# Kernel optimization log

Measured on AMD Instinct MI355X. Metric: run time of the kernel, lower is better.

Reference implementation:

```python
import jax, jax.numpy as jnp
import numpy as np

B, C, H, W = 8, 512, 64, 64
D = C // 8  # 64

def setup_inputs() -> dict:
    key = jax.random.key(0)
    ks = jax.random.split(key, 10)
    s = 0.02
    return {
        "x":  jax.random.normal(ks[0], (B, C, H, W), dtype=jnp.float32),
        "Wq": jax.random.normal(ks[1], (D, C), dtype=jnp.float32) * s,
        "bq": jnp.zeros((D,), dtype=jnp.float32),
        "Wk": jax.random.normal(ks[2], (D, C), dtype=jnp.float32) * s,
        "bk": jnp.zeros((D,), dtype=jnp.float32),
        "Wv": jax.random.normal(ks[3], (D, C), dtype=jnp.float32) * s,
        "bv": jnp.zeros((D,), dtype=jnp.float32),
        "Wo": jax.random.normal(ks[4], (C, D), dtype=jnp.float32) * s,
        "bo": jnp.zeros((C,), dtype=jnp.float32),
        "gamma": jnp.full((1,), 0.5, dtype=jnp.float32),
    }

def reference(x, Wq, bq, Wk, bk, Wv, bv, Wo, bo, gamma):
    b, c, h, w = x.shape
    n = h * w
    xf = x.reshape(b, c, n)                                   # (B, C, N)
    # 1x1 convs == channel matmuls (spectral_norm only reparametrizes the weight)
    q = jnp.einsum('dc,bcn->bnd', Wq, xf) + bq                # (B, N, D)
    k = jnp.einsum('dc,bcn->bdn', Wk, xf) + bk[:, None]       # (B, D, N)
    v = jnp.einsum('dc,bcn->bdn', Wv, xf) + bv[:, None]       # (B, D, N)
    # unscaled scores, softmax over key index (last dim)
    attn = jax.nn.softmax(jnp.einsum('bnd,bdm->bnm', q, k), axis=-1)  # (B, N, N)
    out = jnp.einsum('bdm,bnm->bdn', v, attn)                 # (B, D, N)
    out = jnp.einsum('cd,bdn->bcn', Wo, out) + bo[:, None]    # (B, C, N)
    return (out * gamma + xf).reshape(b, c, h, w)
```

## Files before the change

kernel.cpp:

```cpp
#include <hip/hip_runtime.h>

#define DEVFN __device__ __forceinline__

typedef __bf16 bf16x8 __attribute__((ext_vector_type(8)));
typedef float f32x4 __attribute__((ext_vector_type(4)));
typedef float float4_t __attribute__((ext_vector_type(4)));
typedef unsigned short ushort8_t __attribute__((ext_vector_type(8)));
typedef unsigned short ushort4_t __attribute__((ext_vector_type(4)));

constexpr int Bd = 8, Cd = 512, Nd = 4096, Dd = 64;

DEVFN unsigned short f2bf(float f) {
    union { float f; unsigned int u; } v; v.f = f;
    unsigned int r = (v.u + 0x7FFFu + ((v.u >> 16) & 1u)) >> 16;
    return (unsigned short)r;
}

DEVFN bf16x8 ld_bf8(const unsigned short* p) {
    ushort8_t u = *(const ushort8_t*)p;
    return __builtin_bit_cast(bf16x8, u);
}

DEVFN f32x4 mfma16(bf16x8 a, bf16x8 b, f32x4 c) {
    return __builtin_amdgcn_mfma_f32_16x16x32_bf16(a, b, c, 0, 0, 0);
}

__global__ __launch_bounds__(256) void k_cvtw(
    const float* __restrict__ Wq, const float* __restrict__ Wk,
    const float* __restrict__ Wv, const float* __restrict__ Wo,
    unsigned short* __restrict__ w4)
{
    int i = blockIdx.x * 256 + threadIdx.x;
    w4[i]          = f2bf(Wq[i]);
    w4[32768 + i]  = f2bf(Wk[i]);
    w4[65536 + i]  = f2bf(Wv[i]);
    w4[98304 + i]  = f2bf(Wo[i]);
}

__global__ __launch_bounds__(256) void k_qkv(
    const float* __restrict__ x,
    const unsigned short* __restrict__ wq,
    const unsigned short* __restrict__ wk,
    const unsigned short* __restrict__ wv,
    const float* __restrict__ bq, const float* __restrict__ bk, const float* __restrict__ bv,
    unsigned short* __restrict__ q_nd, unsigned short* __restrict__ k_nd,
    unsigned short* __restrict__ v_dn)
{
    const int b   = blockIdx.y;
    const int n0  = blockIdx.x * 64;
    const int tid = threadIdx.x, wid = tid >> 6, l = tid & 63;
    const int lo  = l & 15, hi = l >> 4;
    const int n0w = n0 + wid * 16;
    const float* xb = x + (size_t)b * Cd * Nd;

    __shared__ unsigned short t_lds[4][16][72];
    __shared__ unsigned short vt_s[64][72];

    f32x4 accq[4] = {}, acck[4] = {}, accv[4] = {};

    for (int c0 = 0; c0 < Cd; c0 += 32) {
        ushort8_t ux;
        #pragma unroll
        for (int j = 0; j < 8; ++j)
            ux[j] = f2bf(xb[(size_t)(c0 + hi * 8 + j) * Nd + n0w + lo]);
        bf16x8 bx = __builtin_bit_cast(bf16x8, ux);
        #pragma unroll
        for (int ds = 0; ds < 4; ++ds) {
            const int wrow = (ds * 16 + lo) * Cd + c0 + hi * 8;
            accq[ds] = mfma16(ld_bf8(wq + wrow), bx, accq[ds]);
            acck[ds] = mfma16(ld_bf8(wk + wrow), bx, acck[ds]);
            accv[ds] = mfma16(ld_bf8(wv + wrow), bx, accv[ds]);
        }
    }

    const int row = l >> 2, dg = l & 3;

    #pragma unroll
    for (int ds = 0; ds < 4; ++ds) {
        ushort4_t u4;
        #pragma unroll
        for (int r = 0; r < 4; ++r) u4[r] = f2bf(accq[ds][r] + bq[ds*16 + hi*4 + r]);
        *(ushort4_t*)&t_lds[wid][lo][ds*16 + hi*4] = u4;
    }
    __syncthreads();
    {
        ushort8_t a0 = *(const ushort8_t*)&t_lds[wid][row][dg*16];
        ushort8_t a1 = *(const ushort8_t*)&t_lds[wid][row][dg*16 + 8];
        unsigned short* dst = q_nd + ((size_t)b * Nd + n0 + wid*16 + row) * 64 + dg*16;
        *(ushort8_t*)dst = a0; *(ushort8_t*)(dst + 8) = a1;
    }
    __syncthreads();

    #pragma unroll
    for (int ds = 0; ds < 4; ++ds) {
        ushort4_t u4;
        #pragma unroll
        for (int r = 0; r < 4; ++r) u4[r] = f2bf(acck[ds][r] + bk[ds*16 + hi*4 + r]);
        *(ushort4_t*)&t_lds[wid][lo][ds*16 + hi*4] = u4;
    }
    __syncthreads();
    {
        ushort8_t a0 = *(const ushort8_t*)&t_lds[wid][row][dg*16];
        ushort8_t a1 = *(const ushort8_t*)&t_lds[wid][row][dg*16 + 8];
        unsigned short* dst = k_nd + ((size_t)b * Nd + n0 + wid*16 + row) * 64 + dg*16;
        *(ushort8_t*)dst = a0; *(ushort8_t*)(dst + 8) = a1;
    }
    __syncthreads();

    #pragma unroll
    for (int ds = 0; ds < 4; ++ds) {
        #pragma unroll
        for (int r = 0; r < 4; ++r)
            vt_s[ds*16 + hi*4 + r][wid*16 + lo] = f2bf(accv[ds][r] + bv[ds*16 + hi*4 + r]);
    }
    __syncthreads();
    {
        const int d = tid >> 2, ng = tid & 3;
        ushort8_t a0 = *(const ushort8_t*)&vt_s[d][ng*16];
        ushort8_t a1 = *(const ushort8_t*)&vt_s[d][ng*16 + 8];
        unsigned short* dst = v_dn + ((size_t)b * Dd + d) * Nd + n0 + ng*16;
        *(ushort8_t*)dst = a0; *(ushort8_t*)(dst + 8) = a1;
    }
}

__global__ __launch_bounds__(256, 2) void k_attn(
    const unsigned short* __restrict__ q_nd,
    const unsigned short* __restrict__ k_nd,
    const unsigned short* __restrict__ v_dn,
    unsigned short* __restrict__ o_nd)
{
    const int bid = blockIdx.x;
    const int b   = bid & 7;
    const int n0  = (bid >> 3) * 64;
    const int tid = threadIdx.x, wid = tid >> 6, l = tid & 63;
    const int lo  = l & 15, hi = l >> 4;
    const int n0w = n0 + wid * 16;
    const int lsw = lo & 7;

    __shared__ unsigned short k_tile[64 * 64];
    __shared__ unsigned short v_tile[64 * 64];
    __shared__ unsigned short p_lds[4][16][72];

    const unsigned short* qb = q_nd + (size_t)b * Nd * Dd;
    const unsigned short* kb = k_nd + (size_t)b * Nd * Dd;
    const unsigned short* vb = v_dn + (size_t)b * Dd * Nd;

    bf16x8 aq[2];
    #pragma unroll
    for (int kc = 0; kc < 2; ++kc)
        aq[kc] = ld_bf8(qb + (size_t)(n0w + lo) * 64 + kc*32 + hi*8);

    f32x4 acc[4] = {};
    float l_st[4] = {0.f, 0.f, 0.f, 0.f};

    const int sr = tid >> 3, ss = tid & 7;
    const int wsl = (ss ^ (sr & 7)) * 8;
    ushort8_t kr0, kr1, vr0, vr1;

    auto gload = [&](int t) {
        const size_t m1 = (size_t)t * 64;
        kr0 = *(const ushort8_t*)(kb + (m1 + sr) * 64 + ss * 8);
        kr1 = *(const ushort8_t*)(kb + (m1 + 32 + sr) * 64 + ss * 8);
        vr0 = *(const ushort8_t*)(vb + (size_t)sr * Nd + m1 + ss * 8);
        vr1 = *(const ushort8_t*)(vb + (size_t)(32 + sr) * Nd + m1 + ss * 8);
    };
    auto dswrite = [&]() {
        *(ushort8_t*)(k_tile + sr * 64 + wsl)        = kr0;
        *(ushort8_t*)(k_tile + (32 + sr) * 64 + wsl) = kr1;
        *(ushort8_t*)(v_tile + sr * 64 + wsl)        = vr0;
        *(ushort8_t*)(v_tile + (32 + sr) * 64 + wsl) = vr1;
    };

    auto compute = [&]() {
        f32x4 s[4] = {};
        #pragma unroll
        for (int ms = 0; ms < 4; ++ms) {
            #pragma unroll
            for (int kc = 0; kc < 2; ++kc) {
                bf16x8 kf = ld_bf8(k_tile + (ms*16 + lo) * 64 + (((kc*4 + hi) ^ lsw) * 8));
                s[ms] = mfma16(aq[kc], kf, s[ms]);
            }
        }
        float p[4][4];
        #pragma unroll
        for (int ms = 0; ms < 4; ++ms) {
            #pragma unroll
            for (int r = 0; r < 4; ++r)
                p[ms][r] = __expf(s[ms][r]);
        }
        #pragma unroll
        for (int r = 0; r < 4; ++r)
            l_st[r] += (p[0][r] + p[1][r]) + (p[2][r] + p[3][r]);
        #pragma unroll
        for (int ms = 0; ms < 4; ++ms) {
            #pragma unroll
            for (int r = 0; r < 4; ++r)
                p_lds[wid][hi*4 + r][ms*16 + lo] = f2bf(p[ms][r]);
        }
        asm volatile("" ::: "memory");
        bf16x8 ap0 = ld_bf8(&p_lds[wid][lo][0*32 + hi*8]);
        bf16x8 ap1 = ld_bf8(&p_lds[wid][lo][1*32 + hi*8]);
        #pragma unroll
        for (int ds = 0; ds < 4; ++ds) {
            bf16x8 vf0 = ld_bf8(v_tile + (ds*16 + lo) * 64 + (((0*4 + hi) ^ lsw) * 8));
            acc[ds] = mfma16(ap0, vf0, acc[ds]);
            bf16x8 vf1 = ld_bf8(v_tile + (ds*16 + lo) * 64 + (((1*4 + hi) ^ lsw) * 8));
            acc[ds] = mfma16(ap1, vf1, acc[ds]);
        }
    };

    constexpr int NT = Nd / 64;
    gload(0);
    dswrite();
    __syncthreads();
    for (int t = 0; t < NT - 1; ++t) {
        gload(t + 1);
        __builtin_amdgcn_sched_barrier(0);
        compute();
        __syncthreads();
        dswrite();
        __syncthreads();
    }
    compute();

    float lr[4];
    #pragma unroll
    for (int r = 0; r < 4; ++r) {
        float ps = l_st[r];
        #pragma unroll
        for (int off = 1; off < 16; off <<= 1)
            ps += __shfl_xor(ps, off, 64);
        lr[r] = ps;
    }
    #pragma unroll
    for (int ds = 0; ds < 4; ++ds) {
        #pragma unroll
        for (int r = 0; r < 4; ++r) {
            float o = acc[ds][r] / lr[r];
            o_nd[((size_t)b * Nd + n0w + hi*4 + r) * 64 + ds*16 + lo] = f2bf(o);
        }
    }
}

__global__ __launch_bounds__(256) void k_oproj(
    const unsigned short* __restrict__ o_nd,
    const unsigned short* __restrict__ wo,
    const float* __restrict__ bo,
    const float* __restrict__ gamma,
    const float* __restrict__ x,
    float* __restrict__ out)
{
    const int b   = blockIdx.y;
    const int n0  = blockIdx.x * 64;
    const int tid = threadIdx.x, wid = tid >> 6, l = tid & 63;
    const int lo  = l & 15, hi = l >> 4;
    const int n0w = n0 + wid * 16;
    const float g = gamma[0];

    bf16x8 ao[2];
    #pragma unroll
    for (int kc = 0; kc < 2; ++kc)
        ao[kc] = ld_bf8(o_nd + ((size_t)b * Nd + n0w + lo) * 64 + kc*32 + hi*8);

    for (int ct = 0; ct < 32; ++ct) {
        f32x4 acc = {};
        #pragma unroll
        for (int kc = 0; kc < 2; ++kc) {
            bf16x8 bw = ld_bf8(wo + (ct*16 + lo) * 64 + kc*32 + hi*8);
            acc = mfma16(ao[kc], bw, acc);
        }
        const int c = ct*16 + lo;
        const float bc = bo[c];
        const size_t base = ((size_t)b * Cd + c) * Nd + n0w + hi*4;
        float4_t xv = *(const float4_t*)(x + base);
        float4_t ov;
        #pragma unroll
        for (int r = 0; r < 4; ++r) ov[r] = g * (acc[r] + bc) + xv[r];
        *(float4_t*)(out + base) = ov;
    }
}

extern "C" void kernel_launch(void* const* d_in, const int* in_sizes, int n_in,
                              void* d_out, int out_size, void* d_ws, size_t ws_size,
                              hipStream_t stream) {
    (void)in_sizes; (void)n_in; (void)out_size; (void)ws_size;
    const float* x  = (const float*)d_in[0];
    const float* Wq = (const float*)d_in[1];
    const float* bq = (const float*)d_in[2];
    const float* Wk = (const float*)d_in[3];
    const float* bk = (const float*)d_in[4];
    const float* Wv = (const float*)d_in[5];
    const float* bv = (const float*)d_in[6];
    const float* Wo = (const float*)d_in[7];
    const float* bo = (const float*)d_in[8];
    const float* gm = (const float*)d_in[9];
    float* out = (float*)d_out;

    unsigned short* w4   = (unsigned short*)d_ws;
    unsigned short* q_nd = w4 + 131072;
    unsigned short* k_nd = q_nd + (size_t)Bd * Nd * Dd;
    unsigned short* v_dn = k_nd + (size_t)Bd * Nd * Dd;
    unsigned short* o_nd = v_dn + (size_t)Bd * Nd * Dd;

    k_cvtw<<<128, 256, 0, stream>>>(Wq, Wk, Wv, Wo, w4);
    dim3 g1(Nd / 64, Bd);
    k_qkv<<<g1, 256, 0, stream>>>(x, w4, w4 + 32768, w4 + 65536, bq, bk, bv, q_nd, k_nd, v_dn);
    k_attn<<<512, 256, 0, stream>>>(q_nd, k_nd, v_dn, o_nd);
    k_oproj<<<g1, 256, 0, stream>>>(o_nd, w4 + 98304, bo, gm, x, out);
}
```

Measured before the change: 169.0 us.

## Restructure attention kernel: register-resident P, 2x2 wave split, double-buffered K/V

Splits the four waves into a 2x2 grid over query halves and key halves, so each K fragment read from LDS feeds two query sub-tiles. Computes S transposed so the exponentiated probabilities can be packed directly into the MFMA A-operand in registers, which removes the P round trip through LDS. Double-buffers the K/V tiles to drop one barrier per iteration, stores V with a permuted swizzle to match the new fragment layout, and adds an LDS cross-wave reduction of partial outputs and row sums at the end. This costs more registers for accumulators and extra LDS for the reduction buffers, which may lower occupancy.

```diff
diff --git a/kernel.cpp b/kernel.cpp
--- a/kernel.cpp
+++ b/kernel.cpp
@@ -1,4 +1,5 @@
 #include <hip/hip_runtime.h>
+#include <hip/hip_bf16.h>
 
 #define DEVFN __device__ __forceinline__
 
@@ -7,6 +8,7 @@
 typedef float float4_t __attribute__((ext_vector_type(4)));
 typedef unsigned short ushort8_t __attribute__((ext_vector_type(8)));
 typedef unsigned short ushort4_t __attribute__((ext_vector_type(4)));
+typedef unsigned int uint4_t __attribute__((ext_vector_type(4)));
 
 constexpr int Bd = 8, Cd = 512, Nd = 4096, Dd = 64;
 
@@ -14,6 +16,12 @@
     union { float f; unsigned int u; } v; v.f = f;
     unsigned int r = (v.u + 0x7FFFu + ((v.u >> 16) & 1u)) >> 16;
     return (unsigned short)r;
+}
+
+DEVFN unsigned int pack2(float a, float b) {
+    __hip_bfloat162 h = __float22bfloat162_rn(make_float2(a, b));
+    union { __hip_bfloat162 h; unsigned int u; } c; c.h = h;
+    return c.u;
 }
 
 DEVFN bf16x8 ld_bf8(const unsigned short* p) {
@@ -134,27 +142,36 @@
     const int n0  = (bid >> 3) * 64;
     const int tid = threadIdx.x, wid = tid >> 6, l = tid & 63;
     const int lo  = l & 15, hi = l >> 4;
-    const int n0w = n0 + wid * 16;
     const int lsw = lo & 7;
-
-    __shared__ unsigned short k_tile[64 * 64];
-    __shared__ unsigned short v_tile[64 * 64];
-    __shared__ unsigned short p_lds[4][16][72];
+    const int qh  = wid >> 1;
+    const int kh  = wid & 1;
+    const int wk0 = kh * 32;
+
+    __shared__ unsigned short k_tiles[2][64 * 64];
+    __shared__ unsigned short v_tiles[2][64 * 64];
+    __shared__ float red_acc[2][2][4][256];
+    __shared__ float red_l[2][2][16];
 
     const unsigned short* qb = q_nd + (size_t)b * Nd * Dd;
     const unsigned short* kb = k_nd + (size_t)b * Nd * Dd;
     const unsigned short* vb = v_dn + (size_t)b * Dd * Nd;
 
-    bf16x8 aq[2];
-    #pragma unroll
-    for (int kc = 0; kc < 2; ++kc)
-        aq[kc] = ld_bf8(qb + (size_t)(n0w + lo) * 64 + kc*32 + hi*8);
-
-    f32x4 acc[4] = {};
-    float l_st[4] = {0.f, 0.f, 0.f, 0.f};
+    bf16x8 aq[2][2];
+    #pragma unroll
+    for (int qs = 0; qs < 2; ++qs)
+        #pragma unroll
+        for (int kc = 0; kc < 2; ++kc)
+            aq[qs][kc] = ld_bf8(qb + (size_t)(n0 + qh*32 + qs*16 + lo) * 64 + kc*32 + hi*8);
+
+    f32x4 acc[2][4] = {};
+    float l_p[2] = {0.f, 0.f};
 
     const int sr = tid >> 3, ss = tid & 7;
-    const int wsl = (ss ^ (sr & 7)) * 8;
+    const int kwsl = (ss ^ (sr & 7)) * 8;
+    const int vkh = ss >> 2, vsl = ss & 3, vms = vsl >> 1;
+    const int vg0 = vkh * 4 + ((2 * vsl) & 3);
+    const int vg1 = vkh * 4 + ((2 * vsl + 1) & 3);
+    const int vsw = sr & 7;
     ushort8_t kr0, kr1, vr0, vr1;
 
     auto gload = [&](int t) {
@@ -164,80 +181,109 @@
         vr0 = *(const ushort8_t*)(vb + (size_t)sr * Nd + m1 + ss * 8);
         vr1 = *(const ushort8_t*)(vb + (size_t)(32 + sr) * Nd + m1 + ss * 8);
     };
-    auto dswrite = [&]() {
-        *(ushort8_t*)(k_tile + sr * 64 + wsl)        = kr0;
-        *(ushort8_t*)(k_tile + (32 + sr) * 64 + wsl) = kr1;
-        *(ushort8_t*)(v_tile + sr * 64 + wsl)        = vr0;
-        *(ushort8_t*)(v_tile + (32 + sr) * 64 + wsl) = vr1;
+    auto dswrite = [&](int buf) {
+        unsigned short* kt = k_tiles[buf];
+        unsigned short* vt = v_tiles[buf];
+        *(ushort8_t*)(kt + sr * 64 + kwsl)        = kr0;
+        *(ushort8_t*)(kt + (32 + sr) * 64 + kwsl) = kr1;
+        ushort4_t a0 = __builtin_shufflevector(vr0, vr0, 0, 1, 2, 3);
+        ushort4_t a1 = __builtin_shufflevector(vr0, vr0, 4, 5, 6, 7);
+        ushort4_t b0 = __builtin_shufflevector(vr1, vr1, 0, 1, 2, 3);
+        ushort4_t b1 = __builtin_shufflevector(vr1, vr1, 4, 5, 6, 7);
+        *(ushort4_t*)(vt + sr * 64 + (vg0 ^ vsw) * 8 + vms * 4)        = a0;
+        *(ushort4_t*)(vt + sr * 64 + (vg1 ^ vsw) * 8 + vms * 4)        = a1;
+        *(ushort4_t*)(vt + (32 + sr) * 64 + (vg0 ^ vsw) * 8 + vms * 4) = b0;
+        *(ushort4_t*)(vt + (32 + sr) * 64 + (vg1 ^ vsw) * 8 + vms * 4) = b1;
     };
 
-    auto compute = [&]() {
-        f32x4 s[4] = {};
-        #pragma unroll
-        for (int ms = 0; ms < 4; ++ms) {
+    auto compute = [&](int buf) {
+        const unsigned short* kt = k_tiles[buf];
+        const unsigned short* vt = v_tiles[buf];
+        f32x4 s[2][2] = {};
+        #pragma unroll
+        for (int ms = 0; ms < 2; ++ms) {
             #pragma unroll
             for (int kc = 0; kc < 2; ++kc) {
-                bf16x8 kf = ld_bf8(k_tile + (ms*16 + lo) * 64 + (((kc*4 + hi) ^ lsw) * 8));
-                s[ms] = mfma16(aq[kc], kf, s[ms]);
+                bf16x8 kf = ld_bf8(kt + (wk0 + ms*16 + lo) * 64 + (((kc*4 + hi) ^ lsw) * 8));
+                #pragma unroll
+                for (int qs = 0; qs < 2; ++qs)
+                    s[qs][ms] = mfma16(kf, aq[qs][kc], s[qs][ms]);
             }
         }
-        float p[4][4];
-        #pragma unroll
-        for (int ms = 0; ms < 4; ++ms) {
-            #pragma unroll
-            for (int r = 0; r < 4; ++r)
-                p[ms][r] = __expf(s[ms][r]);
-        }
-        #pragma unroll
-        for (int r = 0; r < 4; ++r)
-            l_st[r] += (p[0][r] + p[1][r]) + (p[2][r] + p[3][r]);
-        #pragma unroll
-        for (int ms = 0; ms < 4; ++ms) {
-            #pragma unroll
-            for (int r = 0; r < 4; ++r)
-                p_lds[wid][hi*4 + r][ms*16 + lo] = f2bf(p[ms][r]);
-        }
-        asm volatile("" ::: "memory");
-        bf16x8 ap0 = ld_bf8(&p_lds[wid][lo][0*32 + hi*8]);
-        bf16x8 ap1 = ld_bf8(&p_lds[wid][lo][1*32 + hi*8]);
-        #pragma unroll
-        for (int ds = 0; ds < 4; ++ds) {
-            bf16x8 vf0 = ld_bf8(v_tile + (ds*16 + lo) * 64 + (((0*4 + hi) ^ lsw) * 8));
-            acc[ds] = mfma16(ap0, vf0, acc[ds]);
-            bf16x8 vf1 = ld_bf8(v_tile + (ds*16 + lo) * 64 + (((1*4 + hi) ^ lsw) * 8));
-            acc[ds] = mfma16(ap1, vf1, acc[ds]);
+        bf16x8 vf[4];
+        #pragma unroll
+        for (int ds = 0; ds < 4; ++ds)
+            vf[ds] = ld_bf8(vt + (ds*16 + lo) * 64 + (((kh*4 + hi) ^ lsw) * 8));
+        #pragma unroll
+        for (int qs = 0; qs < 2; ++qs) {
+            float p[2][4];
+            #pragma unroll
+            for (int ms = 0; ms < 2; ++ms)
+                #pragma unroll
+                for (int r = 0; r < 4; ++r)
+                    p[ms][r] = __expf(s[qs][ms][r]);
+            l_p[qs] += ((p[0][0] + p[0][1]) + (p[0][2] + p[0][3]))
+                     + ((p[1][0] + p[1][1]) + (p[1][2] + p[1][3]));
+            uint4_t w;
+            w[0] = pack2(p[0][0], p[0][1]);
+            w[1] = pack2(p[0][2], p[0][3]);
+            w[2] = pack2(p[1][0], p[1][1]);
+            w[3] = pack2(p[1][2], p[1][3]);
+            bf16x8 apf = __builtin_bit_cast(bf16x8, w);
+            #pragma unroll
+            for (int ds = 0; ds < 4; ++ds)
+                acc[qs][ds] = mfma16(apf, vf[ds], acc[qs][ds]);
         }
     };
 
     constexpr int NT = Nd / 64;
     gload(0);
-    dswrite();
-    __syncthreads();
-    for (int t = 0; t < NT - 1; ++t) {
-        gload(t + 1);
+    dswrite(0);
+    __syncthreads();
+    for (int t = 0; t < NT; ++t) {
+        const int cur = t & 1;
+        if (t + 1 < NT) gload(t + 1);
         __builtin_amdgcn_sched_barrier(0);
-        compute();
+        compute(cur);
+        if (t + 1 < NT) dswrite(cur ^ 1);
         __syncthreads();
-        dswrite();
-        __syncthreads();
-    }
-    compute();
-
-    float lr[4];
-    #pragma unroll
-    for (int r = 0; r < 4; ++r) {
-        float ps = l_st[r];
-        #pragma unroll
-        for (int off = 1; off < 16; off <<= 1)
-            ps += __shfl_xor(ps, off, 64);
-        lr[r] = ps;
-    }
-    #pragma unroll
-    for (int ds = 0; ds < 4; ++ds) {
-        #pragma unroll
-        for (int r = 0; r < 4; ++r) {
-            float o = acc[ds][r] / lr[r];
-            o_nd[((size_t)b * Nd + n0w + hi*4 + r) * 64 + ds*16 + lo] = f2bf(o);
+    }
+
+    float lh[2];
+    #pragma unroll
+    for (int qs = 0; qs < 2; ++qs) {
+        float ps = l_p[qs];
+        ps += __shfl_xor(ps, 16, 64);
+        ps += __shfl_xor(ps, 32, 64);
+        lh[qs] = ps;
+    }
+    if (kh == 1) {
+        #pragma unroll
+        for (int qs = 0; qs < 2; ++qs) {
+            #pragma unroll
+            for (int ds = 0; ds < 4; ++ds)
+                *(f32x4*)&red_acc[qh][qs][ds][l * 4] = acc[qs][ds];
+            red_l[qh][qs][lo] = lh[qs];
+        }
+    }
+    __syncthreads();
+    if (kh == 0) {
+        #pragma unroll
+        for (int qs = 0; qs < 2; ++qs) {
+            #pragma unroll
+            for (int ds = 0; ds < 4; ++ds)
+                acc[qs][ds] += *(const f32x4*)&red_acc[qh][qs][ds][l * 4];
+            float l_tot = lh[qs] + red_l[qh][qs][lo];
+            #pragma unroll
+            for (int r = 0; r < 4; ++r) {
+                float lq = __shfl(l_tot, hi * 4 + r, 16);
+                float rl = 1.0f / lq;
+                #pragma unroll
+                for (int ds = 0; ds < 4; ++ds) {
+                    float o = acc[qs][ds][r] * rl;
+                    o_nd[((size_t)b * Nd + n0 + qh*32 + qs*16 + hi*4 + r) * 64 + ds*16 + lo] = f2bf(o);
+                }
+            }
         }
     }
 }
```

New measurement: 151.3 us. 10.5% less time.
